# Kernel optimization log

Measured on AMD Instinct MI355X. Metric: run time of the kernel, lower is better.

The kernel has to match this reference:

```python
import jax, jax.numpy as jnp
import numpy as np

N = 100000   # nodes
E = 640000   # directed edges
D = 128      # feature dim
C = 2        # classes


def setup_inputs() -> dict:
    key = jax.random.key(0)
    ks = jax.random.split(key, 7)
    s = 1.0 / np.sqrt(D)
    return {
        "x": jax.random.normal(ks[0], (N, D), jnp.float32),
        "edge_index": jax.random.randint(ks[1], (2, E), 0, N, jnp.int32),
        "W1": jax.random.normal(ks[2], (D, D), jnp.float32) * s,
        "b1": jnp.zeros((D,), jnp.float32),
        "W2": jax.random.normal(ks[3], (D, D), jnp.float32) * s,
        "b2": jnp.zeros((D,), jnp.float32),
        "Wfc": jax.random.normal(ks[4], (D, C), jnp.float32) * s,
        "bfc": jnp.zeros((C,), jnp.float32),
    }


def _gcn_conv(h, src, dst, W, b, n):
    """PyG GCNConv: y = D^{-1/2}(A+I)D^{-1/2} (h @ W) + b."""
    h = h @ W  # [N, D_out]
    loop = jnp.arange(n, dtype=src.dtype)
    s = jnp.concatenate([src, loop])
    d = jnp.concatenate([dst, loop])
    # degree of (A + I) counted at destination
    deg = jax.ops.segment_sum(jnp.ones_like(d, jnp.float32), d, num_segments=n)
    dinv = jax.lax.rsqrt(jnp.maximum(deg, 1.0))  # deg >= 1 via self loops
    norm = dinv[s] * dinv[d]                      # [E+N]
    msg = h[s] * norm[:, None]                    # gather + scale
    out = jax.ops.segment_sum(msg, d, num_segments=n)  # scatter-add
    return out + b


def reference(x, edge_index, W1, b1, W2, b2, Wfc, bfc):
    src, dst = edge_index[0], edge_index[1]
    n = x.shape[0]
    h = jax.nn.relu(_gcn_conv(x, src, dst, W1, b1, n))  # dropout = identity (eval)
    h = jax.nn.relu(_gcn_conv(h, src, dst, W2, b2, n))
    return h @ Wfc + bfc  # [N, 2] logits
```

## Files before the change

### kernel.cpp

```cpp
#include <hip/hip_runtime.h>
#include <hip/hip_bf16.h>

#define D 128

typedef __bf16 bf16x8 __attribute__((ext_vector_type(8)));
typedef float f32x4 __attribute__((ext_vector_type(4)));



__global__ void count_kernel(const int* __restrict__ dst, int* __restrict__ counts,
                             int* __restrict__ eoff, int e) {
    int i0 = (blockIdx.x * 256 + threadIdx.x) * 4;
    if (i0 + 4 <= e) {
        int4 d4 = *(const int4*)(dst + i0);
        int4 o;
        o.x = atomicAdd(&counts[d4.x], 1);
        o.y = atomicAdd(&counts[d4.y], 1);
        o.z = atomicAdd(&counts[d4.z], 1);
        o.w = atomicAdd(&counts[d4.w], 1);
        *(int4*)(eoff + i0) = o;
    } else {
        for (int i = i0; i < e; i++) eoff[i] = atomicAdd(&counts[dst[i]], 1);
    }
}

__global__ void dinv_kernel(const int* __restrict__ counts, float* __restrict__ dinv, int n) {
    int i = blockIdx.x * 256 + threadIdx.x;
    if (i < n) dinv[i] = rsqrtf((float)(counts[i] + 1));
}

__global__ void scan_part(const int* __restrict__ counts, int* __restrict__ partial, int n) {
    __shared__ int sm[256];
    int b = blockIdx.x, t = threadIdx.x;
    int base = b * 2048 + t * 8;
    int s = 0;
#pragma unroll
    for (int j = 0; j < 8; j++) { int idx = base + j; if (idx < n) s += counts[idx]; }
    sm[t] = s; __syncthreads();
    for (int off = 128; off > 0; off >>= 1) { if (t < off) sm[t] += sm[t + off]; __syncthreads(); }
    if (t == 0) partial[b] = sm[0];
}

__global__ void scan_top(int* partial, int nb) {
    __shared__ int sm[256];
    int t = threadIdx.x;
    int v = (t < nb) ? partial[t] : 0;
    sm[t] = v; __syncthreads();
    for (int off = 1; off < 256; off <<= 1) {
        int u = (t >= off) ? sm[t - off] : 0;
        __syncthreads();
        sm[t] += u;
        __syncthreads();
    }
    if (t < nb) partial[t] = sm[t] - v;
}

__global__ void scan_down(const int* __restrict__ counts, const int* __restrict__ blockoff,
                          int* __restrict__ row_ptr, int n) {
    __shared__ int sm[256];
    int b = blockIdx.x, t = threadIdx.x;
    int base = b * 2048 + t * 8;
    int c[8], local[8];
    int s = 0;
#pragma unroll
    for (int j = 0; j < 8; j++) {
        int idx = base + j;
        c[j] = (idx < n) ? counts[idx] : 0;
        local[j] = s; s += c[j];
    }
    sm[t] = s; __syncthreads();
    int own = s;
    for (int off = 1; off < 256; off <<= 1) {
        int u = (t >= off) ? sm[t - off] : 0;
        __syncthreads();
        sm[t] += u;
        __syncthreads();
    }
    int basev = blockoff[b] + sm[t] - own;
#pragma unroll
    for (int j = 0; j < 8; j++) { int idx = base + j; if (idx < n) row_ptr[idx] = basev + local[j]; }
}

__global__ void fill_kernel(const int* __restrict__ src, const int* __restrict__ dst,
                            const int* __restrict__ row_ptr, const int* __restrict__ eoff,
                            const float* __restrict__ dinv, int2* __restrict__ csr, int e) {
    int i0 = (blockIdx.x * 256 + threadIdx.x) * 4;
    if (i0 + 4 <= e) {
        int4 s4 = *(const int4*)(src + i0);
        int4 d4 = *(const int4*)(dst + i0);
        int4 o4 = *(const int4*)(eoff + i0);
        int p0 = row_ptr[d4.x] + o4.x;
        int p1 = row_ptr[d4.y] + o4.y;
        int p2 = row_ptr[d4.z] + o4.z;
        int p3 = row_ptr[d4.w] + o4.w;
        float w0 = dinv[s4.x] * dinv[d4.x];
        float w1 = dinv[s4.y] * dinv[d4.y];
        float w2 = dinv[s4.z] * dinv[d4.z];
        float w3 = dinv[s4.w] * dinv[d4.w];
        csr[p0] = make_int2(s4.x, __float_as_int(w0));
        csr[p1] = make_int2(s4.y, __float_as_int(w1));
        csr[p2] = make_int2(s4.z, __float_as_int(w2));
        csr[p3] = make_int2(s4.w, __float_as_int(w3));
    } else {
        for (int i = i0; i < e; i++) {
            int s = src[i], d = dst[i];
            int pos = row_ptr[d] + eoff[i];
            csr[pos] = make_int2(s, __float_as_int(dinv[s] * dinv[d]));
        }
    }
}


__global__ void pack_w(const float* __restrict__ W1, const float* __restrict__ W2,
                       __bf16* __restrict__ pw) {
    int t = blockIdx.x * 256 + threadIdx.x;
    int which = t >> 14, idx = t & 16383;
    const float* W = which ? W2 : W1;
    float w = W[idx];
    int k = idx >> 7, n = idx & 127;
    int ks = which ? (((k & 15) << 3) | (k >> 4)) : k;
    int ntile = n >> 4, nl = n & 15;
    int kchunk = ks >> 5, quad = (ks >> 3) & 3, j = ks & 7;
    int o = (((ntile * 4 + kchunk) * 64 + quad * 16 + nl) << 3) + j;
    pw[(size_t)which * 16384 + o] = (__bf16)w;
}


__global__ void gemm1_mfma(const float* __restrict__ X, const __bf16* __restrict__ PW,
                           __bf16* __restrict__ Zs, int nrows) {
    __shared__ bf16x8 sB[2048];
    int t = threadIdx.x;
    const bf16x8* PW8 = (const bf16x8*)PW;
#pragma unroll
    for (int i = 0; i < 8; i++) sB[t + 256 * i] = PW8[t + 256 * i];

    int wave = t >> 6, lane = t & 63;
    int qm = lane & 15, quad = lane >> 4;
    int r0 = blockIdx.x * 64 + wave * 16;
    int row = r0 + qm;
    bool valid = row < nrows;
    const float* xr = X + (size_t)row * D + quad * 8;

    bf16x8 ahi[4], alo[4];
#pragma unroll
    for (int c = 0; c < 4; c++) {
        float4 zf = {0.f, 0.f, 0.f, 0.f};
        float4 xa = valid ? ((const float4*)(xr + c * 32))[0] : zf;
        float4 xb = valid ? ((const float4*)(xr + c * 32))[1] : zf;
        float xs[8] = {xa.x, xa.y, xa.z, xa.w, xb.x, xb.y, xb.z, xb.w};
        bf16x8 h, l;
#pragma unroll
        for (int j = 0; j < 8; j++) {
            float v = xs[j];
            __bf16 hh = (__bf16)v;
            h[j] = hh;
            l[j] = (__bf16)(v - (float)hh);
        }
        ahi[c] = h; alo[c] = l;
    }

    f32x4 acc[8];
#pragma unroll
    for (int nt = 0; nt < 8; nt++) acc[nt] = (f32x4){0.f, 0.f, 0.f, 0.f};

    __syncthreads();

#pragma unroll
    for (int c = 0; c < 4; c++) {
#pragma unroll
        for (int nt = 0; nt < 8; nt++) {
            bf16x8 b = sB[(nt * 4 + c) * 64 + lane];
            acc[nt] = __builtin_amdgcn_mfma_f32_16x16x32_bf16(ahi[c], b, acc[nt], 0, 0, 0);
            acc[nt] = __builtin_amdgcn_mfma_f32_16x16x32_bf16(alo[c], b, acc[nt], 0, 0, 0);
        }
    }

#pragma unroll
    for (int reg = 0; reg < 4; reg++) {
        int orow = r0 + quad * 4 + reg;
        if (orow < nrows) {
            bf16x8 o;
#pragma unroll
            for (int nt = 0; nt < 8; nt++) o[nt] = (__bf16)acc[nt][reg];
            *(bf16x8*)(Zs + (size_t)orow * D + qm * 8) = o;
        }
    }
}


__global__ void gemm2_mfma(const __bf16* __restrict__ Hs, const __bf16* __restrict__ PW,
                           __bf16* __restrict__ Zs, int nrows) {
    __shared__ bf16x8 sB[2048];
    int t = threadIdx.x;
    const bf16x8* PW8 = (const bf16x8*)PW;
#pragma unroll
    for (int i = 0; i < 8; i++) sB[t + 256 * i] = PW8[t + 256 * i];

    int wave = t >> 6, lane = t & 63;
    int qm = lane & 15, quad = lane >> 4;
    int r0 = blockIdx.x * 64 + wave * 16;
    int row = r0 + qm;
    bool valid = row < nrows;
    const __bf16* hr = Hs + (size_t)row * D + quad * 8;

    bf16x8 a[4];
#pragma unroll
    for (int c = 0; c < 4; c++) {
        bf16x8 z8 = {};
        a[c] = valid ? *(const bf16x8*)(hr + c * 32) : z8;
    }

    f32x4 acc[8];
#pragma unroll
    for (int nt = 0; nt < 8; nt++) acc[nt] = (f32x4){0.f, 0.f, 0.f, 0.f};

    __syncthreads();

#pragma unroll
    for (int c = 0; c < 4; c++) {
#pragma unroll
        for (int nt = 0; nt < 8; nt++) {
            bf16x8 b = sB[(nt * 4 + c) * 64 + lane];
            acc[nt] = __builtin_amdgcn_mfma_f32_16x16x32_bf16(a[c], b, acc[nt], 0, 0, 0);
        }
    }

#pragma unroll
    for (int reg = 0; reg < 4; reg++) {
        int orow = r0 + quad * 4 + reg;
        if (orow < nrows) {
            bf16x8 o;
#pragma unroll
            for (int nt = 0; nt < 8; nt++) o[nt] = (__bf16)acc[nt][reg];
            *(bf16x8*)(Zs + (size_t)orow * D + qm * 8) = o;
        }
    }
}


__global__ void agg1_kernel(const __bf16* __restrict__ Zs, const int* __restrict__ row_ptr,
                            const int* __restrict__ counts, const int2* __restrict__ csr,
                            const float* __restrict__ dinv, const float* __restrict__ bias,
                            __bf16* __restrict__ Hs, int n) {
    int t = blockIdx.x * 256 + threadIdx.x;
    int v = t >> 4, c = t & 15;
    if (v >= n) return;
    float dv = dinv[v];
    const bf16x8* Z8 = (const bf16x8*)Zs;
    bf16x8 zc = Z8[(size_t)v * 16 + c];
    float sw = dv * dv;
    float acc[8];
#pragma unroll
    for (int j = 0; j < 8; j++) acc[j] = (float)zc[j] * sw;
    int start = row_ptr[v], cnt = counts[v];
    int i = 0;
    for (; i + 4 <= cnt; i += 4) {
        int2 e0 = csr[start + i], e1 = csr[start + i + 1];
        int2 e2 = csr[start + i + 2], e3 = csr[start + i + 3];
        bf16x8 m0 = Z8[(size_t)e0.x * 16 + c];
        bf16x8 m1 = Z8[(size_t)e1.x * 16 + c];
        bf16x8 m2 = Z8[(size_t)e2.x * 16 + c];
        bf16x8 m3 = Z8[(size_t)e3.x * 16 + c];
        float w0 = __int_as_float(e0.y), w1 = __int_as_float(e1.y);
        float w2 = __int_as_float(e2.y), w3 = __int_as_float(e3.y);
#pragma unroll
        for (int j = 0; j < 8; j++) acc[j] = fmaf(w0, (float)m0[j], acc[j]);
#pragma unroll
        for (int j = 0; j < 8; j++) acc[j] = fmaf(w1, (float)m1[j], acc[j]);
#pragma unroll
        for (int j = 0; j < 8; j++) acc[j] = fmaf(w2, (float)m2[j], acc[j]);
#pragma unroll
        for (int j = 0; j < 8; j++) acc[j] = fmaf(w3, (float)m3[j], acc[j]);
    }
    for (; i < cnt; i++) {
        int2 e0 = csr[start + i];
        float w0 = __int_as_float(e0.y);
        bf16x8 m0 = Z8[(size_t)e0.x * 16 + c];
#pragma unroll
        for (int j = 0; j < 8; j++) acc[j] = fmaf(w0, (float)m0[j], acc[j]);
    }
    bf16x8 o;
#pragma unroll
    for (int j = 0; j < 8; j++) o[j] = (__bf16)fmaxf(acc[j] + bias[j * 16 + c], 0.f);
    ((bf16x8*)Hs)[(size_t)v * 16 + c] = o;
}


__global__ void agg2_fc_kernel(const __bf16* __restrict__ Zs, const int* __restrict__ row_ptr,
                               const int* __restrict__ counts, const int2* __restrict__ csr,
                               const float* __restrict__ dinv, const float* __restrict__ bias,
                               const float* __restrict__ Wfc, const float* __restrict__ bfc,
                               float* __restrict__ out, int n) {
    int t = blockIdx.x * 256 + threadIdx.x;
    int v = t >> 4, c = t & 15;
    if (v >= n) return;
    float dv = dinv[v];
    const bf16x8* Z8 = (const bf16x8*)Zs;
    bf16x8 zc = Z8[(size_t)v * 16 + c];
    float sw = dv * dv;
    float acc[8];
#pragma unroll
    for (int j = 0; j < 8; j++) acc[j] = (float)zc[j] * sw;
    int start = row_ptr[v], cnt = counts[v];
    int i = 0;
    for (; i + 4 <= cnt; i += 4) {
        int2 e0 = csr[start + i], e1 = csr[start + i + 1];
        int2 e2 = csr[start + i + 2], e3 = csr[start + i + 3];
        bf16x8 m0 = Z8[(size_t)e0.x * 16 + c];
        bf16x8 m1 = Z8[(size_t)e1.x * 16 + c];
        bf16x8 m2 = Z8[(size_t)e2.x * 16 + c];
        bf16x8 m3 = Z8[(size_t)e3.x * 16 + c];
        float w0 = __int_as_float(e0.y), w1 = __int_as_float(e1.y);
        float w2 = __int_as_float(e2.y), w3 = __int_as_float(e3.y);
#pragma unroll
        for (int j = 0; j < 8; j++) acc[j] = fmaf(w0, (float)m0[j], acc[j]);
#pragma unroll
        for (int j = 0; j < 8; j++) acc[j] = fmaf(w1, (float)m1[j], acc[j]);
#pragma unroll
        for (int j = 0; j < 8; j++) acc[j] = fmaf(w2, (float)m2[j], acc[j]);
#pragma unroll
        for (int j = 0; j < 8; j++) acc[j] = fmaf(w3, (float)m3[j], acc[j]);
    }
    for (; i < cnt; i++) {
        int2 e0 = csr[start + i];
        float w0 = __int_as_float(e0.y);
        bf16x8 m0 = Z8[(size_t)e0.x * 16 + c];
#pragma unroll
        for (int j = 0; j < 8; j++) acc[j] = fmaf(w0, (float)m0[j], acc[j]);
    }
    float a0 = 0.f, a1 = 0.f;
#pragma unroll
    for (int j = 0; j < 8; j++) {
        int p = j * 16 + c;
        float hj = fmaxf(acc[j] + bias[p], 0.f);
        a0 = fmaf(hj, Wfc[p * 2], a0);
        a1 = fmaf(hj, Wfc[p * 2 + 1], a1);
    }
#pragma unroll
    for (int off = 8; off > 0; off >>= 1) {
        a0 += __shfl_down(a0, off, 16);
        a1 += __shfl_down(a1, off, 16);
    }
    if (c == 0) {
        out[(size_t)v * 2 + 0] = a0 + bfc[0];
        out[(size_t)v * 2 + 1] = a1 + bfc[1];
    }
}


extern "C" void kernel_launch(void* const* d_in, const int* in_sizes, int n_in,
                              void* d_out, int out_size, void* d_ws, size_t ws_size,
                              hipStream_t stream) {
    const float* x   = (const float*)d_in[0];
    const int*   ei  = (const int*)d_in[1];
    const float* W1  = (const float*)d_in[2];
    const float* b1  = (const float*)d_in[3];
    const float* W2  = (const float*)d_in[4];
    const float* b2  = (const float*)d_in[5];
    const float* Wfc = (const float*)d_in[6];
    const float* bfc = (const float*)d_in[7];
    float* out = (float*)d_out;

    int n = in_sizes[0] / D;
    int e = in_sizes[1] / 2;
    const int* src = ei;
    const int* dst = ei + e;

    char* ws = (char*)d_ws;
    size_t nb = (size_t)n * 4;
    int*    counts  = (int*)(ws);
    float*  dinv    = (float*)(ws + nb);
    int*    rowptr  = (int*)(ws + 2 * nb);
    int*    partial = (int*)(ws + 3 * nb);
    int*    eoff    = (int*)(ws + 3 * nb + 1024);
    int2*   csr     = (int2*)(ws + 3 * nb + 1024 + (size_t)e * 4);
    __bf16* pw      = (__bf16*)(ws + 3 * nb + 1024 + (size_t)e * 12);
    __bf16* z1      = (__bf16*)(ws + 3 * nb + 1024 + (size_t)e * 12 + 65536);
    __bf16* h1      = z1 + (size_t)n * D;
    __bf16* z2      = h1 + (size_t)n * D;

    hipMemsetAsync(counts, 0, nb, stream);

    int e4b = (e / 4 + 255) / 256 + 1;
    int sb = (n + 2047) / 2048;
    int gb = (n + 63) / 64;
    int ab = ((n * 16) + 255) / 256;

    count_kernel<<<e4b, 256, 0, stream>>>(dst, counts, eoff, e);
    dinv_kernel<<<(n + 255) / 256, 256, 0, stream>>>(counts, dinv, n);
    scan_part<<<sb, 256, 0, stream>>>(counts, partial, n);
    scan_top<<<1, 256, 0, stream>>>(partial, sb);
    scan_down<<<sb, 256, 0, stream>>>(counts, partial, rowptr, n);
    fill_kernel<<<e4b, 256, 0, stream>>>(src, dst, rowptr, eoff, dinv, csr, e);
    pack_w<<<128, 256, 0, stream>>>(W1, W2, pw);

    gemm1_mfma<<<gb, 256, 0, stream>>>(x, pw, z1, n);
    agg1_kernel<<<ab, 256, 0, stream>>>(z1, rowptr, counts, csr, dinv, b1, h1, n);
    gemm2_mfma<<<gb, 256, 0, stream>>>(h1, pw + 16384, z2, n);
    agg2_fc_kernel<<<ab, 256, 0, stream>>>(z2, rowptr, counts, csr, dinv, b2, Wfc, bfc, out, n);
}
```

Measured before the change: 251.3 us.

## Fuse preprocessing launches and use single-pass decoupled scan for CSR build

Merges the memset, weight packing and control init into one prep kernel, and replaces the three-kernel scan plus the dinv kernel with one fused scan. The fused scan takes chunks in order through an atomic ticket and chains prefixes through flags. Count and fill kernels now handle 8 edges per thread, and the aggregation kernels gain an 8-way unrolled gather loop for more memory-level parallelism. The aim is fewer kernel launches and less launch and sync overhead. The cost is a serial spin-wait chain across scan blocks and higher register pressure in the aggregation kernels.

```diff
diff --git a/kernel.cpp b/kernel.cpp
--- a/kernel.cpp
+++ b/kernel.cpp
@@ -8,58 +8,68 @@
 
 
 
+__global__ void prep_kernel(const float* __restrict__ W1, const float* __restrict__ W2,
+                            __bf16* __restrict__ pw, int* __restrict__ counts,
+                            int* __restrict__ ctrl, int n, int nzb) {
+    int b = blockIdx.x;
+    if (b < 128) {
+        int t = b * 256 + threadIdx.x;
+        int which = t >> 14, idx = t & 16383;
+        const float* W = which ? W2 : W1;
+        float w = W[idx];
+        int k = idx >> 7, nn = idx & 127;
+        int ks = which ? (((k & 15) << 3) | (k >> 4)) : k;
+        int ntile = nn >> 4, nl = nn & 15;
+        int kchunk = ks >> 5, quad = (ks >> 3) & 3, j = ks & 7;
+        int o = (((ntile * 4 + kchunk) * 64 + quad * 16 + nl) << 3) + j;
+        pw[(size_t)which * 16384 + o] = (__bf16)w;
+    } else if (b < 128 + nzb) {
+        int i0 = (b - 128) * 1024 + threadIdx.x * 4;
+        if (i0 + 4 <= n) {
+            *(int4*)(counts + i0) = make_int4(0, 0, 0, 0);
+        } else {
+            for (int i = i0; i < n; i++) counts[i] = 0;
+        }
+    } else {
+        int t = threadIdx.x;
+        if (t == 0) ctrl[0] = 0;
+        if (t < 64) ctrl[1 + t] = -1;
+    }
+}
+
+
 __global__ void count_kernel(const int* __restrict__ dst, int* __restrict__ counts,
                              int* __restrict__ eoff, int e) {
-    int i0 = (blockIdx.x * 256 + threadIdx.x) * 4;
-    if (i0 + 4 <= e) {
-        int4 d4 = *(const int4*)(dst + i0);
-        int4 o;
-        o.x = atomicAdd(&counts[d4.x], 1);
-        o.y = atomicAdd(&counts[d4.y], 1);
-        o.z = atomicAdd(&counts[d4.z], 1);
-        o.w = atomicAdd(&counts[d4.w], 1);
-        *(int4*)(eoff + i0) = o;
+    int i0 = (blockIdx.x * 256 + threadIdx.x) * 8;
+    if (i0 + 8 <= e) {
+        int4 a = *(const int4*)(dst + i0);
+        int4 b = *(const int4*)(dst + i0 + 4);
+        int4 oa, ob;
+        oa.x = atomicAdd(&counts[a.x], 1);
+        oa.y = atomicAdd(&counts[a.y], 1);
+        oa.z = atomicAdd(&counts[a.z], 1);
+        oa.w = atomicAdd(&counts[a.w], 1);
+        ob.x = atomicAdd(&counts[b.x], 1);
+        ob.y = atomicAdd(&counts[b.y], 1);
+        ob.z = atomicAdd(&counts[b.z], 1);
+        ob.w = atomicAdd(&counts[b.w], 1);
+        *(int4*)(eoff + i0) = oa;
+        *(int4*)(eoff + i0 + 4) = ob;
     } else {
         for (int i = i0; i < e; i++) eoff[i] = atomicAdd(&counts[dst[i]], 1);
     }
 }
 
-__global__ void dinv_kernel(const int* __restrict__ counts, float* __restrict__ dinv, int n) {
-    int i = blockIdx.x * 256 + threadIdx.x;
-    if (i < n) dinv[i] = rsqrtf((float)(counts[i] + 1));
-}
-
-__global__ void scan_part(const int* __restrict__ counts, int* __restrict__ partial, int n) {
+
+__global__ void scan_fused(const int* __restrict__ counts, float* __restrict__ dinv,
+                           int* __restrict__ row_ptr, int* __restrict__ ctrl, int n) {
     __shared__ int sm[256];
-    int b = blockIdx.x, t = threadIdx.x;
-    int base = b * 2048 + t * 8;
-    int s = 0;
-#pragma unroll
-    for (int j = 0; j < 8; j++) { int idx = base + j; if (idx < n) s += counts[idx]; }
-    sm[t] = s; __syncthreads();
-    for (int off = 128; off > 0; off >>= 1) { if (t < off) sm[t] += sm[t + off]; __syncthreads(); }
-    if (t == 0) partial[b] = sm[0];
-}
-
-__global__ void scan_top(int* partial, int nb) {
-    __shared__ int sm[256];
+    __shared__ int schunk, sbase;
     int t = threadIdx.x;
-    int v = (t < nb) ? partial[t] : 0;
-    sm[t] = v; __syncthreads();
-    for (int off = 1; off < 256; off <<= 1) {
-        int u = (t >= off) ? sm[t - off] : 0;
-        __syncthreads();
-        sm[t] += u;
-        __syncthreads();
-    }
-    if (t < nb) partial[t] = sm[t] - v;
-}
-
-__global__ void scan_down(const int* __restrict__ counts, const int* __restrict__ blockoff,
-                          int* __restrict__ row_ptr, int n) {
-    __shared__ int sm[256];
-    int b = blockIdx.x, t = threadIdx.x;
-    int base = b * 2048 + t * 8;
+    if (t == 0) schunk = atomicAdd(&ctrl[0], 1);
+    __syncthreads();
+    int chunk = schunk;
+    int base = chunk * 2048 + t * 8;
     int c[8], local[8];
     int s = 0;
 #pragma unroll
@@ -67,6 +77,7 @@
         int idx = base + j;
         c[j] = (idx < n) ? counts[idx] : 0;
         local[j] = s; s += c[j];
+        if (idx < n) dinv[idx] = rsqrtf((float)(c[j] + 1));
     }
     sm[t] = s; __syncthreads();
     int own = s;
@@ -76,31 +87,44 @@
         sm[t] += u;
         __syncthreads();
     }
-    int basev = blockoff[b] + sm[t] - own;
+    if (t == 0) {
+        int prev = 0;
+        if (chunk > 0) {
+            while ((prev = __hip_atomic_load(&ctrl[1 + chunk - 1], __ATOMIC_ACQUIRE,
+                                             __HIP_MEMORY_SCOPE_AGENT)) < 0) {}
+        }
+        sbase = prev;
+        __hip_atomic_store(&ctrl[1 + chunk], prev + sm[255], __ATOMIC_RELEASE,
+                           __HIP_MEMORY_SCOPE_AGENT);
+    }
+    __syncthreads();
+    int basev = sbase + sm[t] - own;
 #pragma unroll
     for (int j = 0; j < 8; j++) { int idx = base + j; if (idx < n) row_ptr[idx] = basev + local[j]; }
 }
+
 
 __global__ void fill_kernel(const int* __restrict__ src, const int* __restrict__ dst,
                             const int* __restrict__ row_ptr, const int* __restrict__ eoff,
                             const float* __restrict__ dinv, int2* __restrict__ csr, int e) {
-    int i0 = (blockIdx.x * 256 + threadIdx.x) * 4;
-    if (i0 + 4 <= e) {
-        int4 s4 = *(const int4*)(src + i0);
-        int4 d4 = *(const int4*)(dst + i0);
-        int4 o4 = *(const int4*)(eoff + i0);
-        int p0 = row_ptr[d4.x] + o4.x;
-        int p1 = row_ptr[d4.y] + o4.y;
-        int p2 = row_ptr[d4.z] + o4.z;
-        int p3 = row_ptr[d4.w] + o4.w;
-        float w0 = dinv[s4.x] * dinv[d4.x];
-        float w1 = dinv[s4.y] * dinv[d4.y];
-        float w2 = dinv[s4.z] * dinv[d4.z];
-        float w3 = dinv[s4.w] * dinv[d4.w];
-        csr[p0] = make_int2(s4.x, __float_as_int(w0));
-        csr[p1] = make_int2(s4.y, __float_as_int(w1));
-        csr[p2] = make_int2(s4.z, __float_as_int(w2));
-        csr[p3] = make_int2(s4.w, __float_as_int(w3));
+    int i0 = (blockIdx.x * 256 + threadIdx.x) * 8;
+    if (i0 + 8 <= e) {
+        int4 sa = *(const int4*)(src + i0);
+        int4 sb = *(const int4*)(src + i0 + 4);
+        int4 da = *(const int4*)(dst + i0);
+        int4 db = *(const int4*)(dst + i0 + 4);
+        int4 oa = *(const int4*)(eoff + i0);
+        int4 ob = *(const int4*)(eoff + i0 + 4);
+        int sv[8] = {sa.x, sa.y, sa.z, sa.w, sb.x, sb.y, sb.z, sb.w};
+        int dv[8] = {da.x, da.y, da.z, da.w, db.x, db.y, db.z, db.w};
+        int ov[8] = {oa.x, oa.y, oa.z, oa.w, ob.x, ob.y, ob.z, ob.w};
+        int p[8]; float ww[8];
+#pragma unroll
+        for (int u = 0; u < 8; u++) p[u] = row_ptr[dv[u]] + ov[u];
+#pragma unroll
+        for (int u = 0; u < 8; u++) ww[u] = dinv[sv[u]] * dinv[dv[u]];
+#pragma unroll
+        for (int u = 0; u < 8; u++) csr[p[u]] = make_int2(sv[u], __float_as_int(ww[u]));
     } else {
         for (int i = i0; i < e; i++) {
             int s = src[i], d = dst[i];
@@ -108,21 +132,6 @@
             csr[pos] = make_int2(s, __float_as_int(dinv[s] * dinv[d]));
         }
     }
-}
-
-
-__global__ void pack_w(const float* __restrict__ W1, const float* __restrict__ W2,
-                       __bf16* __restrict__ pw) {
-    int t = blockIdx.x * 256 + threadIdx.x;
-    int which = t >> 14, idx = t & 16383;
-    const float* W = which ? W2 : W1;
-    float w = W[idx];
-    int k = idx >> 7, n = idx & 127;
-    int ks = which ? (((k & 15) << 3) | (k >> 4)) : k;
-    int ntile = n >> 4, nl = n & 15;
-    int kchunk = ks >> 5, quad = (ks >> 3) & 3, j = ks & 7;
-    int o = (((ntile * 4 + kchunk) * 64 + quad * 16 + nl) << 3) + j;
-    pw[(size_t)which * 16384 + o] = (__bf16)w;
 }
 
 
@@ -254,6 +263,19 @@
     for (int j = 0; j < 8; j++) acc[j] = (float)zc[j] * sw;
     int start = row_ptr[v], cnt = counts[v];
     int i = 0;
+    for (; i + 8 <= cnt; i += 8) {
+        int2 ee[8]; bf16x8 mm[8];
+#pragma unroll
+        for (int u = 0; u < 8; u++) ee[u] = csr[start + i + u];
+#pragma unroll
+        for (int u = 0; u < 8; u++) mm[u] = Z8[(size_t)ee[u].x * 16 + c];
+#pragma unroll
+        for (int u = 0; u < 8; u++) {
+            float w = __int_as_float(ee[u].y);
+#pragma unroll
+            for (int j = 0; j < 8; j++) acc[j] = fmaf(w, (float)mm[u][j], acc[j]);
+        }
+    }
     for (; i + 4 <= cnt; i += 4) {
         int2 e0 = csr[start + i], e1 = csr[start + i + 1];
         int2 e2 = csr[start + i + 2], e3 = csr[start + i + 3];
@@ -303,6 +325,19 @@
     for (int j = 0; j < 8; j++) acc[j] = (float)zc[j] * sw;
     int start = row_ptr[v], cnt = counts[v];
     int i = 0;
+    for (; i + 8 <= cnt; i += 8) {
+        int2 ee[8]; bf16x8 mm[8];
+#pragma unroll
+        for (int u = 0; u < 8; u++) ee[u] = csr[start + i + u];
+#pragma unroll
+        for (int u = 0; u < 8; u++) mm[u] = Z8[(size_t)ee[u].x * 16 + c];
+#pragma unroll
+        for (int u = 0; u < 8; u++) {
+            float w = __int_as_float(ee[u].y);
+#pragma unroll
+            for (int j = 0; j < 8; j++) acc[j] = fmaf(w, (float)mm[u][j], acc[j]);
+        }
+    }
     for (; i + 4 <= cnt; i += 4) {
         int2 e0 = csr[start + i], e1 = csr[start + i + 1];
         int2 e2 = csr[start + i + 2], e3 = csr[start + i + 3];
@@ -371,7 +406,7 @@
     int*    counts  = (int*)(ws);
     float*  dinv    = (float*)(ws + nb);
     int*    rowptr  = (int*)(ws + 2 * nb);
-    int*    partial = (int*)(ws + 3 * nb);
+    int*    ctrl    = (int*)(ws + 3 * nb);
     int*    eoff    = (int*)(ws + 3 * nb + 1024);
     int2*   csr     = (int2*)(ws + 3 * nb + 1024 + (size_t)e * 4);
     __bf16* pw      = (__bf16*)(ws + 3 * nb + 1024 + (size_t)e * 12);
@@ -379,20 +414,16 @@
     __bf16* h1      = z1 + (size_t)n * D;
     __bf16* z2      = h1 + (size_t)n * D;
 
-    hipMemsetAsync(counts, 0, nb, stream);
-
-    int e4b = (e / 4 + 255) / 256 + 1;
-    int sb = (n + 2047) / 2048;
-    int gb = (n + 63) / 64;
-    int ab = ((n * 16) + 255) / 256;
-
-    count_kernel<<<e4b, 256, 0, stream>>>(dst, counts, eoff, e);
-    dinv_kernel<<<(n + 255) / 256, 256, 0, stream>>>(counts, dinv, n);
-    scan_part<<<sb, 256, 0, stream>>>(counts, partial, n);
-    scan_top<<<1, 256, 0, stream>>>(partial, sb);
-    scan_down<<<sb, 256, 0, stream>>>(counts, partial, rowptr, n);
-    fill_kernel<<<e4b, 256, 0, stream>>>(src, dst, rowptr, eoff, dinv, csr, e);
-    pack_w<<<128, 256, 0, stream>>>(W1, W2, pw);
+    int nzb = (n + 1023) / 1024;
+    int e8b = ((e + 7) / 8 + 255) / 256;
+    int scb = (n + 2047) / 2048;
+    int gb  = (n + 63) / 64;
+    int ab  = ((n * 16) + 255) / 256;
+
+    prep_kernel<<<128 + nzb + 1, 256, 0, stream>>>(W1, W2, pw, counts, ctrl, n, nzb);
+    count_kernel<<<e8b, 256, 0, stream>>>(dst, counts, eoff, e);
+    scan_fused<<<scb, 256, 0, stream>>>(counts, dinv, rowptr, ctrl, n);
+    fill_kernel<<<e8b, 256, 0, stream>>>(src, dst, rowptr, eoff, dinv, csr, e);
 
     gemm1_mfma<<<gb, 256, 0, stream>>>(x, pw, z1, n);
     agg1_kernel<<<ab, 256, 0, stream>>>(z1, rowptr, counts, csr, dinv, b1, h1, n);
```

Result: slower. 302.9 us (+20.6%).

## Fuse launch chain: merge pack_w with counts zeroing and gemm1 with degree counting

Applied to the files above, without the earlier changes.

The hipMemsetAsync and pack_w launches are replaced by one prep kernel that packs weights in some blocks and zeroes the counts array in others. The first GEMM and the edge-degree counting atomics now share a single launch, with different block ranges doing each job so the two run concurrently. dinv is computed inside scan_down, which removes the separate dinv kernel. This cuts four launches and their serialization gaps. The cost is that the GEMM blocks may share the GPU with atomic-heavy blocks, and the fused kernel reserves the GEMM's shared memory even for counting blocks.

```diff
diff --git a/kernel.cpp b/kernel.cpp
--- a/kernel.cpp
+++ b/kernel.cpp
@@ -8,26 +8,110 @@
 
 
 
-__global__ void count_kernel(const int* __restrict__ dst, int* __restrict__ counts,
+__global__ void prep_kernel(const float* __restrict__ W1, const float* __restrict__ W2,
+                            __bf16* __restrict__ pw, int* __restrict__ counts, int n) {
+    int b = blockIdx.x;
+    if (b < 128) {
+        int t = b * 256 + threadIdx.x;
+        int which = t >> 14, idx = t & 16383;
+        const float* W = which ? W2 : W1;
+        float w = W[idx];
+        int k = idx >> 7, nn = idx & 127;
+        int ks = which ? (((k & 15) << 3) | (k >> 4)) : k;
+        int ntile = nn >> 4, nl = nn & 15;
+        int kchunk = ks >> 5, quad = (ks >> 3) & 3, j = ks & 7;
+        int o = (((ntile * 4 + kchunk) * 64 + quad * 16 + nl) << 3) + j;
+        pw[(size_t)which * 16384 + o] = (__bf16)w;
+    } else {
+        int i0 = (b - 128) * 1024 + threadIdx.x * 4;
+        if (i0 + 4 <= n) {
+            *(int4*)(counts + i0) = make_int4(0, 0, 0, 0);
+        } else {
+            for (int i = i0; i < n; i++) counts[i] = 0;
+        }
+    }
+}
+
+
+__global__ void mega1_kernel(const float* __restrict__ X, const __bf16* __restrict__ PW,
+                             __bf16* __restrict__ Zs, int nrows, int gb,
+                             const int* __restrict__ dst, int* __restrict__ counts,
                              int* __restrict__ eoff, int e) {
-    int i0 = (blockIdx.x * 256 + threadIdx.x) * 4;
-    if (i0 + 4 <= e) {
-        int4 d4 = *(const int4*)(dst + i0);
-        int4 o;
-        o.x = atomicAdd(&counts[d4.x], 1);
-        o.y = atomicAdd(&counts[d4.y], 1);
-        o.z = atomicAdd(&counts[d4.z], 1);
-        o.w = atomicAdd(&counts[d4.w], 1);
-        *(int4*)(eoff + i0) = o;
-    } else {
-        for (int i = i0; i < e; i++) eoff[i] = atomicAdd(&counts[dst[i]], 1);
-    }
-}
-
-__global__ void dinv_kernel(const int* __restrict__ counts, float* __restrict__ dinv, int n) {
-    int i = blockIdx.x * 256 + threadIdx.x;
-    if (i < n) dinv[i] = rsqrtf((float)(counts[i] + 1));
-}
+    __shared__ bf16x8 sB[2048];
+    int b = blockIdx.x;
+    if (b >= gb) {
+        int i0 = ((b - gb) * 256 + threadIdx.x) * 4;
+        if (i0 + 4 <= e) {
+            int4 d4 = *(const int4*)(dst + i0);
+            int4 o;
+            o.x = atomicAdd(&counts[d4.x], 1);
+            o.y = atomicAdd(&counts[d4.y], 1);
+            o.z = atomicAdd(&counts[d4.z], 1);
+            o.w = atomicAdd(&counts[d4.w], 1);
+            *(int4*)(eoff + i0) = o;
+        } else {
+            for (int i = i0; i < e; i++) eoff[i] = atomicAdd(&counts[dst[i]], 1);
+        }
+        return;
+    }
+    int t = threadIdx.x;
+    const bf16x8* PW8 = (const bf16x8*)PW;
+#pragma unroll
+    for (int i = 0; i < 8; i++) sB[t + 256 * i] = PW8[t + 256 * i];
+
+    int wave = t >> 6, lane = t & 63;
+    int qm = lane & 15, quad = lane >> 4;
+    int r0 = b * 64 + wave * 16;
+    int row = r0 + qm;
+    bool valid = row < nrows;
+    const float* xr = X + (size_t)row * D + quad * 8;
+
+    bf16x8 ahi[4], alo[4];
+#pragma unroll
+    for (int c = 0; c < 4; c++) {
+        float4 zf = {0.f, 0.f, 0.f, 0.f};
+        float4 xa = valid ? ((const float4*)(xr + c * 32))[0] : zf;
+        float4 xb = valid ? ((const float4*)(xr + c * 32))[1] : zf;
+        float xs[8] = {xa.x, xa.y, xa.z, xa.w, xb.x, xb.y, xb.z, xb.w};
+        bf16x8 h, l;
+#pragma unroll
+        for (int j = 0; j < 8; j++) {
+            float v = xs[j];
+            __bf16 hh = (__bf16)v;
+            h[j] = hh;
+            l[j] = (__bf16)(v - (float)hh);
+        }
+        ahi[c] = h; alo[c] = l;
+    }
+
+    f32x4 acc[8];
+#pragma unroll
+    for (int nt = 0; nt < 8; nt++) acc[nt] = (f32x4){0.f, 0.f, 0.f, 0.f};
+
+    __syncthreads();
+
+#pragma unroll
+    for (int c = 0; c < 4; c++) {
+#pragma unroll
+        for (int nt = 0; nt < 8; nt++) {
+            bf16x8 bb = sB[(nt * 4 + c) * 64 + lane];
+            acc[nt] = __builtin_amdgcn_mfma_f32_16x16x32_bf16(ahi[c], bb, acc[nt], 0, 0, 0);
+            acc[nt] = __builtin_amdgcn_mfma_f32_16x16x32_bf16(alo[c], bb, acc[nt], 0, 0, 0);
+        }
+    }
+
+#pragma unroll
+    for (int reg = 0; reg < 4; reg++) {
+        int orow = r0 + quad * 4 + reg;
+        if (orow < nrows) {
+            bf16x8 o;
+#pragma unroll
+            for (int nt = 0; nt < 8; nt++) o[nt] = (__bf16)acc[nt][reg];
+            *(bf16x8*)(Zs + (size_t)orow * D + qm * 8) = o;
+        }
+    }
+}
+
 
 __global__ void scan_part(const int* __restrict__ counts, int* __restrict__ partial, int n) {
     __shared__ int sm[256];
@@ -56,7 +140,7 @@
 }
 
 __global__ void scan_down(const int* __restrict__ counts, const int* __restrict__ blockoff,
-                          int* __restrict__ row_ptr, int n) {
+                          int* __restrict__ row_ptr, float* __restrict__ dinv, int n) {
     __shared__ int sm[256];
     int b = blockIdx.x, t = threadIdx.x;
     int base = b * 2048 + t * 8;
@@ -67,6 +151,7 @@
         int idx = base + j;
         c[j] = (idx < n) ? counts[idx] : 0;
         local[j] = s; s += c[j];
+        if (idx < n) dinv[idx] = rsqrtf((float)(c[j] + 1));
     }
     sm[t] = s; __syncthreads();
     int own = s;
@@ -80,6 +165,7 @@
 #pragma unroll
     for (int j = 0; j < 8; j++) { int idx = base + j; if (idx < n) row_ptr[idx] = basev + local[j]; }
 }
+
 
 __global__ void fill_kernel(const int* __restrict__ src, const int* __restrict__ dst,
                             const int* __restrict__ row_ptr, const int* __restrict__ eoff,
@@ -111,83 +197,6 @@
 }
 
 
-__global__ void pack_w(const float* __restrict__ W1, const float* __restrict__ W2,
-                       __bf16* __restrict__ pw) {
-    int t = blockIdx.x * 256 + threadIdx.x;
-    int which = t >> 14, idx = t & 16383;
-    const float* W = which ? W2 : W1;
-    float w = W[idx];
-    int k = idx >> 7, n = idx & 127;
-    int ks = which ? (((k & 15) << 3) | (k >> 4)) : k;
-    int ntile = n >> 4, nl = n & 15;
-    int kchunk = ks >> 5, quad = (ks >> 3) & 3, j = ks & 7;
-    int o = (((ntile * 4 + kchunk) * 64 + quad * 16 + nl) << 3) + j;
-    pw[(size_t)which * 16384 + o] = (__bf16)w;
-}
-
-
-__global__ void gemm1_mfma(const float* __restrict__ X, const __bf16* __restrict__ PW,
-                           __bf16* __restrict__ Zs, int nrows) {
-    __shared__ bf16x8 sB[2048];
-    int t = threadIdx.x;
-    const bf16x8* PW8 = (const bf16x8*)PW;
-#pragma unroll
-    for (int i = 0; i < 8; i++) sB[t + 256 * i] = PW8[t + 256 * i];
-
-    int wave = t >> 6, lane = t & 63;
-    int qm = lane & 15, quad = lane >> 4;
-    int r0 = blockIdx.x * 64 + wave * 16;
-    int row = r0 + qm;
-    bool valid = row < nrows;
-    const float* xr = X + (size_t)row * D + quad * 8;
-
-    bf16x8 ahi[4], alo[4];
-#pragma unroll
-    for (int c = 0; c < 4; c++) {
-        float4 zf = {0.f, 0.f, 0.f, 0.f};
-        float4 xa = valid ? ((const float4*)(xr + c * 32))[0] : zf;
-        float4 xb = valid ? ((const float4*)(xr + c * 32))[1] : zf;
-        float xs[8] = {xa.x, xa.y, xa.z, xa.w, xb.x, xb.y, xb.z, xb.w};
-        bf16x8 h, l;
-#pragma unroll
-        for (int j = 0; j < 8; j++) {
-            float v = xs[j];
-            __bf16 hh = (__bf16)v;
-            h[j] = hh;
-            l[j] = (__bf16)(v - (float)hh);
-        }
-        ahi[c] = h; alo[c] = l;
-    }
-
-    f32x4 acc[8];
-#pragma unroll
-    for (int nt = 0; nt < 8; nt++) acc[nt] = (f32x4){0.f, 0.f, 0.f, 0.f};
-
-    __syncthreads();
-
-#pragma unroll
-    for (int c = 0; c < 4; c++) {
-#pragma unroll
-        for (int nt = 0; nt < 8; nt++) {
-            bf16x8 b = sB[(nt * 4 + c) * 64 + lane];
-            acc[nt] = __builtin_amdgcn_mfma_f32_16x16x32_bf16(ahi[c], b, acc[nt], 0, 0, 0);
-            acc[nt] = __builtin_amdgcn_mfma_f32_16x16x32_bf16(alo[c], b, acc[nt], 0, 0, 0);
-        }
-    }
-
-#pragma unroll
-    for (int reg = 0; reg < 4; reg++) {
-        int orow = r0 + quad * 4 + reg;
-        if (orow < nrows) {
-            bf16x8 o;
-#pragma unroll
-            for (int nt = 0; nt < 8; nt++) o[nt] = (__bf16)acc[nt][reg];
-            *(bf16x8*)(Zs + (size_t)orow * D + qm * 8) = o;
-        }
-    }
-}
-
-
 __global__ void gemm2_mfma(const __bf16* __restrict__ Hs, const __bf16* __restrict__ PW,
                            __bf16* __restrict__ Zs, int nrows) {
     __shared__ bf16x8 sB[2048];
@@ -379,22 +388,19 @@
     __bf16* h1      = z1 + (size_t)n * D;
     __bf16* z2      = h1 + (size_t)n * D;
 
-    hipMemsetAsync(counts, 0, nb, stream);
-
-    int e4b = (e / 4 + 255) / 256 + 1;
-    int sb = (n + 2047) / 2048;
-    int gb = (n + 63) / 64;
-    int ab = ((n * 16) + 255) / 256;
-
-    count_kernel<<<e4b, 256, 0, stream>>>(dst, counts, eoff, e);
-    dinv_kernel<<<(n + 255) / 256, 256, 0, stream>>>(counts, dinv, n);
+    int nzb = (n + 1023) / 1024;
+    int e4b = ((e + 3) / 4 + 255) / 256;
+    int sb  = (n + 2047) / 2048;
+    int gb  = (n + 63) / 64;
+    int ab  = ((n * 16) + 255) / 256;
+
+    prep_kernel<<<128 + nzb, 256, 0, stream>>>(W1, W2, pw, counts, n);
+    mega1_kernel<<<gb + e4b, 256, 0, stream>>>(x, pw, z1, n, gb, dst, counts, eoff, e);
     scan_part<<<sb, 256, 0, stream>>>(counts, partial, n);
     scan_top<<<1, 256, 0, stream>>>(partial, sb);
-    scan_down<<<sb, 256, 0, stream>>>(counts, partial, rowptr, n);
+    scan_down<<<sb, 256, 0, stream>>>(counts, partial, rowptr, dinv, n);
     fill_kernel<<<e4b, 256, 0, stream>>>(src, dst, rowptr, eoff, dinv, csr, e);
-    pack_w<<<128, 256, 0, stream>>>(W1, W2, pw);
-
-    gemm1_mfma<<<gb, 256, 0, stream>>>(x, pw, z1, n);
+
     agg1_kernel<<<ab, 256, 0, stream>>>(z1, rowptr, counts, csr, dinv, b1, h1, n);
     gemm2_mfma<<<gb, 256, 0, stream>>>(h1, pw + 16384, z2, n);
     agg2_fc_kernel<<<ab, 256, 0, stream>>>(z2, rowptr, counts, csr, dinv, b2, Wfc, bfc, out, n);
```

Result: faster. 240.6 us (-4.3%).
